# Performance work log

Hardware: AMD Instinct MI355X
Metric: run time of the kernel (lower is better)

Reference implementation:

```python
import jax, jax.numpy as jnp
import numpy as np

D_MODEL = 1024
NUM_HEADS = 16
D_FF = 4096
EPS = 1e-5


def _linear(x, w, b):
    # torch nn.Linear: y = x @ W^T + b, W is [out, in]
    return jnp.einsum('bld,od->blo', x, w) + b


def _layer_norm(x, g, b):
    mu = jnp.mean(x, axis=-1, keepdims=True)
    var = jnp.mean(jnp.square(x - mu), axis=-1, keepdims=True)
    return (x - mu) / jnp.sqrt(var + EPS) * g + b


def _mha(q, k, v, wq, bq, wk, bk, wv, bv, wo, bo, mask, num_heads):
    B, Lq, D = q.shape
    hd = D // num_heads
    Q = _linear(q, wq, bq).reshape(B, Lq, num_heads, hd).transpose(0, 2, 1, 3)
    K = _linear(k, wk, bk).reshape(B, -1, num_heads, hd).transpose(0, 2, 1, 3)
    V = _linear(v, wv, bv).reshape(B, -1, num_heads, hd).transpose(0, 2, 1, 3)
    scale = jnp.sqrt(jnp.asarray(hd, dtype=q.dtype))
    energy = jnp.einsum('bhqd,bhkd->bhqk', Q, K) / scale  # [B,H,Lq,Lk]
    energy = jnp.where(mask, energy, jnp.asarray(-1e10, dtype=q.dtype))
    attn = jax.nn.softmax(energy, axis=-1)
    x = jnp.einsum('bhqk,bhkd->bhqd', attn, V)
    x = x.transpose(0, 2, 1, 3).reshape(B, Lq, D)
    return _linear(x, wo, bo), attn


def setup_inputs() -> dict:
    key = jax.random.key(0)
    ks = iter(jax.random.split(key, 40))
    B, T, S, D, F = 4, 1024, 1024, D_MODEL, D_FF
    inp = {
        'tgt': jax.random.normal(next(ks), (B, T, D), dtype=jnp.float32),
        'enc_src': jax.random.normal(next(ks), (B, S, D), dtype=jnp.float32),
        'tgt_mask': jnp.tril(jnp.ones((1, 1, T, T), dtype=bool)),
        'src_mask': jnp.ones((1, 1, 1, S), dtype=bool),
    }
    def lin(kk, o, i):
        return jax.random.normal(kk, (o, i), dtype=jnp.float32) * 0.02
    for pfx in ('sa', 'ca'):  # self-attn and cross-attn params
        for nm in ('q', 'k', 'v', 'o'):
            inp[f'{pfx}_w{nm}'] = lin(next(ks), D, D)
            inp[f'{pfx}_b{nm}'] = jnp.zeros((D,), dtype=jnp.float32)
    inp['ff_w1'] = lin(next(ks), F, D)
    inp['ff_b1'] = jnp.zeros((F,), dtype=jnp.float32)
    inp['ff_w2'] = lin(next(ks), D, F)
    inp['ff_b2'] = jnp.zeros((D,), dtype=jnp.float32)
    for i in (1, 2, 3):
        inp[f'ln{i}_g'] = jnp.ones((D,), dtype=jnp.float32)
        inp[f'ln{i}_b'] = jnp.zeros((D,), dtype=jnp.float32)
    return inp


def reference(tgt, enc_src, tgt_mask, src_mask,
              sa_wq, sa_bq, sa_wk, sa_bk, sa_wv, sa_bv, sa_wo, sa_bo,
              ca_wq, ca_bq, ca_wk, ca_bk, ca_wv, ca_bv, ca_wo, ca_bo,
              ff_w1, ff_b1, ff_w2, ff_b2,
              ln1_g, ln1_b, ln2_g, ln2_b, ln3_g, ln3_b):
    # dropout in eval mode (identity)
    _t, _ = _mha(tgt, tgt, tgt, sa_wq, sa_bq, sa_wk, sa_bk, sa_wv, sa_bv,
                 sa_wo, sa_bo, tgt_mask, NUM_HEADS)
    tgt = _layer_norm(tgt + _t, ln1_g, ln1_b)
    _t, attention = _mha(tgt, enc_src, enc_src, ca_wq, ca_bq, ca_wk, ca_bk,
                         ca_wv, ca_bv, ca_wo, ca_bo, src_mask, NUM_HEADS)
    tgt = _layer_norm(tgt + _t, ln2_g, ln2_b)
    _t = _linear(jax.nn.relu(_linear(tgt, ff_w1, ff_b1)), ff_w2, ff_b2)
    tgt = _layer_norm(tgt + _t, ln3_g, ln3_b)
    return tgt, attention
```

## Files before the change

### kernel.cpp

```cpp
#include <hip/hip_runtime.h>
#include <hip/hip_bf16.h>

#define BBATCH 4
#define TT 1024
#define SS 1024
#define DD 1024
#define HH 16
#define HD 64
#define FFD 4096
#define MM (BBATCH*TT)

using f32x4  = __attribute__((ext_vector_type(4))) float;
using s16x8  = __attribute__((ext_vector_type(8))) short;
using bf16x8 = __attribute__((ext_vector_type(8))) __bf16;

__device__ __forceinline__ unsigned short f2b(float f) {
  union { float f; unsigned int u; } x{f};
  unsigned int r = x.u + 0x7FFFu + ((x.u >> 16) & 1u);
  return (unsigned short)(r >> 16);
}

__device__ __forceinline__ void gload16(const void* g, void* l) {
  __builtin_amdgcn_global_load_lds(
      (const __attribute__((address_space(1))) void*)g,
      (__attribute__((address_space(3))) void*)l, 16, 0, 0);
}

__device__ __forceinline__ f32x4 mfma_bf16(s16x8 a, s16x8 b, f32x4 c) {
  return __builtin_amdgcn_mfma_f32_16x16x32_bf16(
      __builtin_bit_cast(bf16x8, a), __builtin_bit_cast(bf16x8, b), c, 0, 0, 0);
}

template <int JT>
__device__ __forceinline__ void gemm_core(
    const unsigned short* __restrict__ Ab, int lda,
    const unsigned short* __restrict__ Bb, int ldb,
    int K, unsigned short* As, unsigned short* Bs, f32x4 (&acc)[4][JT])
{
  const int tid = threadIdx.x, wave = tid >> 6, lane = tid & 63;
  const int r0 = tid >> 2, c0 = (tid & 3) * 8;
  const int wrow = (wave >> 1) * 64, wcol = (wave & 1) * 16 * JT;
  const int q = lane >> 4, rl = lane & 15;
  const s16x8* Av = (const s16x8*)As;
  const s16x8* Bv = (const s16x8*)Bs;

  for (int k0 = 0; k0 < K; k0 += 32) {
    gload16(Ab + (size_t)r0 * lda + k0 + c0, As + wave * 512);
    gload16(Ab + (size_t)(r0 + 64) * lda + k0 + c0, As + wave * 512 + 2048);
    gload16(Bb + (size_t)r0 * ldb + k0 + c0, Bs + wave * 512);
    if (JT == 4)
      gload16(Bb + (size_t)(r0 + 64) * ldb + k0 + c0, Bs + wave * 512 + 2048);
    __syncthreads();
    s16x8 af[4], bfr[JT];
#pragma unroll
    for (int t = 0; t < 4; t++) af[t] = Av[(wrow + t * 16 + rl) * 4 + q];
#pragma unroll
    for (int t = 0; t < JT; t++) bfr[t] = Bv[(wcol + t * 16 + rl) * 4 + q];
#pragma unroll
    for (int i = 0; i < 4; i++)
#pragma unroll
      for (int j = 0; j < JT; j++)
        acc[i][j] = mfma_bf16(af[i], bfr[j], acc[i][j]);
    __syncthreads();
  }
}

template <int EPI, int JT>
__global__ __launch_bounds__(256) void gemm_bt(
    const unsigned short* __restrict__ A, int lda,
    const unsigned short* __restrict__ B, int ldb,
    const float* __restrict__ bias, const float* __restrict__ res,
    float* __restrict__ Cf, unsigned short* __restrict__ Cb, int ldc, int K)
{
  __shared__ __align__(16) unsigned short As[128 * 32];
  __shared__ __align__(16) unsigned short Bs[JT * 1024];
  const int bm = blockIdx.y, bn = blockIdx.x;
  const int lane = threadIdx.x & 63, wave = threadIdx.x >> 6;
  const int wrow = (wave >> 1) * 64, wcol = (wave & 1) * 16 * JT;
  const int q = lane >> 4, rl = lane & 15;

  f32x4 acc[4][JT];
  f32x4 z = {0.f, 0.f, 0.f, 0.f};
#pragma unroll
  for (int i = 0; i < 4; i++)
#pragma unroll
    for (int j = 0; j < JT; j++) acc[i][j] = z;

  gemm_core<JT>(A + (size_t)bm * 128 * lda, lda,
                B + (size_t)bn * (32 * JT) * ldb, ldb, K, As, Bs, acc);

#pragma unroll
  for (int i = 0; i < 4; i++) {
    int gm0 = bm * 128 + wrow + i * 16 + q * 4;
#pragma unroll
    for (int j = 0; j < JT; j++) {
      int gn = bn * (32 * JT) + wcol + j * 16 + rl;
      float bv = bias[gn];
#pragma unroll
      for (int r = 0; r < 4; r++) {
        size_t off = (size_t)(gm0 + r) * ldc + gn;
        float v = acc[i][j][r];
        if constexpr (EPI == 0) Cb[off] = f2b(v + bv);
        else if constexpr (EPI == 2) Cf[off] = v + bv + res[off];
        else Cb[off] = f2b(fmaxf(v + bv, 0.f));
      }
    }
  }
}

__device__ __forceinline__ void sblock_qk(
    const unsigned short* Qs, const unsigned short* Ks,
    int wrow, int wcol, int q, int rl, f32x4 (&acc)[4][4])
{
  const s16x8* Qv = (const s16x8*)Qs;
  const s16x8* Kv = (const s16x8*)Ks;
  f32x4 z = {0.f, 0.f, 0.f, 0.f};
#pragma unroll
  for (int i = 0; i < 4; i++)
#pragma unroll
    for (int j = 0; j < 4; j++) acc[i][j] = z;
#pragma unroll
  for (int kq = 0; kq < 2; kq++) {
    s16x8 af[4], bf[4];
#pragma unroll
    for (int t = 0; t < 4; t++) af[t] = Qv[kq * 512 + (wrow + t * 16 + rl) * 4 + q];
#pragma unroll
    for (int t = 0; t < 4; t++) bf[t] = Kv[kq * 512 + (wcol + t * 16 + rl) * 4 + q];
#pragma unroll
    for (int i = 0; i < 4; i++)
#pragma unroll
      for (int j = 0; j < 4; j++)
        acc[i][j] = mfma_bf16(af[i], bf[j], acc[i][j]);
  }
}

template <bool CAUSAL, bool WRITE_P>
__global__ __launch_bounds__(256, 2) void flash_attn(
    const unsigned short* __restrict__ Qg, int ldq,
    const unsigned short* __restrict__ Kg, int ldk,
    const unsigned short* __restrict__ Vt,
    float* __restrict__ Pout,
    unsigned short* __restrict__ Og)
{
  __shared__ __align__(16) unsigned short Qs[2 * 128 * 32];
  __shared__ __align__(16) unsigned short KP[4 * 128 * 40];
  __shared__ __align__(16) unsigned short Vs[4 * 64 * 32];
  __shared__ float red[2][128];

  const int tid = threadIdx.x, wave = tid >> 6, lane = tid & 63;
  const int q = lane >> 4, rl = lane & 15;
  const int bm = blockIdx.x, bh = blockIdx.y, b = bh >> 4, h = bh & 15;
  const int wrow = (wave >> 1) * 64, wcol = (wave & 1) * 64;
  const int r0 = tid >> 2, c0 = (tid & 3) * 8;

  const unsigned short* Qbase = Qg + ((size_t)b * TT + bm * 128) * ldq + h * HD;
  const unsigned short* Kbase = Kg + (size_t)b * SS * ldk + h * HD;
  const unsigned short* Vbase = Vt + ((size_t)bh << 16);

#pragma unroll
  for (int kq = 0; kq < 2; kq++) {
    gload16(Qbase + (size_t)r0 * ldq + kq * 32 + c0, Qs + kq * 4096 + wave * 512);
    gload16(Qbase + (size_t)(r0 + 64) * ldq + kq * 32 + c0, Qs + kq * 4096 + wave * 512 + 2048);
  }
  const int nch = CAUSAL ? bm + 1 : 8;
  const float NEG = -3.0e38f;

  float m_run[4][4], l_run[4][4];
#pragma unroll
  for (int i = 0; i < 4; i++)
#pragma unroll
    for (int r = 0; r < 4; r++) { m_run[i][r] = NEG; l_run[i][r] = 0.f; }

  for (int c = 0; c < nch; c++) {
    const unsigned short* src = Kbase + (size_t)c * 128 * ldk;
#pragma unroll
    for (int kq = 0; kq < 2; kq++) {
      gload16(src + (size_t)r0 * ldk + kq * 32 + c0, KP + kq * 4096 + wave * 512);
      gload16(src + (size_t)(r0 + 64) * ldk + kq * 32 + c0, KP + kq * 4096 + wave * 512 + 2048);
    }
    __syncthreads();
    f32x4 acc[4][4];
    sblock_qk(Qs, KP, wrow, wcol, q, rl, acc);
#pragma unroll
    for (int i = 0; i < 4; i++)
#pragma unroll
      for (int j = 0; j < 4; j++)
#pragma unroll
        for (int r = 0; r < 4; r++) {
          float v = acc[i][j][r] * 0.125f;
          if (CAUSAL && c == bm && (wcol + j * 16 + rl) > (wrow + i * 16 + q * 4 + r)) v = NEG;
          acc[i][j][r] = v;
        }
    float mx[4][4];
#pragma unroll
    for (int i = 0; i < 4; i++)
#pragma unroll
      for (int r = 0; r < 4; r++) {
        float m0 = fmaxf(fmaxf(acc[i][0][r], acc[i][1][r]), fmaxf(acc[i][2][r], acc[i][3][r]));
#pragma unroll
        for (int off = 1; off < 16; off <<= 1) m0 = fmaxf(m0, __shfl_xor(m0, off));
        mx[i][r] = m0;
      }
    if (rl == 0) {
#pragma unroll
      for (int i = 0; i < 4; i++)
#pragma unroll
        for (int r = 0; r < 4; r++)
          red[wave & 1][wrow + i * 16 + q * 4 + r] = mx[i][r];
    }
    __syncthreads();
    float mn[4][4];
#pragma unroll
    for (int i = 0; i < 4; i++)
#pragma unroll
      for (int r = 0; r < 4; r++) {
        int row = wrow + i * 16 + q * 4 + r;
        mn[i][r] = fmaxf(m_run[i][r], fmaxf(red[0][row], red[1][row]));
      }
    float cs[4][4];
#pragma unroll
    for (int i = 0; i < 4; i++)
#pragma unroll
      for (int r = 0; r < 4; r++) {
        float s = __expf(acc[i][0][r] - mn[i][r]) + __expf(acc[i][1][r] - mn[i][r]) +
                  __expf(acc[i][2][r] - mn[i][r]) + __expf(acc[i][3][r] - mn[i][r]);
#pragma unroll
        for (int off = 1; off < 16; off <<= 1) s += __shfl_xor(s, off);
        cs[i][r] = s;
      }
    __syncthreads();
    if (rl == 0) {
#pragma unroll
      for (int i = 0; i < 4; i++)
#pragma unroll
        for (int r = 0; r < 4; r++)
          red[wave & 1][wrow + i * 16 + q * 4 + r] = cs[i][r];
    }
    __syncthreads();
#pragma unroll
    for (int i = 0; i < 4; i++)
#pragma unroll
      for (int r = 0; r < 4; r++) {
        int row = wrow + i * 16 + q * 4 + r;
        float tot = red[0][row] + red[1][row];
        l_run[i][r] = l_run[i][r] * __expf(m_run[i][r] - mn[i][r]) + tot;
        m_run[i][r] = mn[i][r];
      }
    __syncthreads();
  }

  float invl[4][4];
#pragma unroll
  for (int i = 0; i < 4; i++)
#pragma unroll
    for (int r = 0; r < 4; r++) invl[i][r] = 1.0f / l_run[i][r];

  const int wc2 = (wave & 1) * 32;
  f32x4 oacc[4][2];
  f32x4 z = {0.f, 0.f, 0.f, 0.f};
#pragma unroll
  for (int i = 0; i < 4; i++) { oacc[i][0] = z; oacc[i][1] = z; }

  for (int c = 0; c < nch; c++) {
    __syncthreads();
    const unsigned short* src = Kbase + (size_t)c * 128 * ldk;
#pragma unroll
    for (int kq = 0; kq < 2; kq++) {
      gload16(src + (size_t)r0 * ldk + kq * 32 + c0, KP + kq * 4096 + wave * 512);
      gload16(src + (size_t)(r0 + 64) * ldk + kq * 32 + c0, KP + kq * 4096 + wave * 512 + 2048);
    }
#pragma unroll
    for (int ks = 0; ks < 4; ks++)
      gload16(Vbase + (size_t)r0 * SS + c * 128 + ks * 32 + c0, Vs + ks * 2048 + wave * 512);
    __syncthreads();
    f32x4 acc[4][4];
    sblock_qk(Qs, KP, wrow, wcol, q, rl, acc);
#pragma unroll
    for (int i = 0; i < 4; i++)
#pragma unroll
      for (int j = 0; j < 4; j++)
#pragma unroll
        for (int r = 0; r < 4; r++) {
          float v = acc[i][j][r] * 0.125f;
          bool msk = CAUSAL && c == bm && (wcol + j * 16 + rl) > (wrow + i * 16 + q * 4 + r);
          acc[i][j][r] = msk ? 0.f : __expf(v - m_run[i][r]) * invl[i][r];
        }
    if (WRITE_P) {
      float* Pb = Pout + ((size_t)bh << 20) +
                  ((size_t)(bm * 128 + wrow + q * 4) << 10) + c * 128 + wcol + rl;
#pragma unroll
      for (int i = 0; i < 4; i++)
#pragma unroll
        for (int r = 0; r < 4; r++)
#pragma unroll
          for (int j = 0; j < 4; j++)
            Pb[(size_t)((i * 16 + r) << 10) + j * 16] = acc[i][j][r];
    }
    __syncthreads();
#pragma unroll
    for (int i = 0; i < 4; i++)
#pragma unroll
      for (int j = 0; j < 4; j++) {
        int col = wcol + j * 16 + rl;
        int ks = col >> 5, cc = col & 31;
#pragma unroll
        for (int r = 0; r < 4; r++)
          KP[ks * 5120 + (wrow + i * 16 + q * 4 + r) * 40 + cc] = f2b(acc[i][j][r]);
      }
    __syncthreads();
    const s16x8* Pv = (const s16x8*)KP;
    const s16x8* Vv = (const s16x8*)Vs;
#pragma unroll
    for (int ks = 0; ks < 4; ks++) {
      s16x8 af[4], bf[2];
#pragma unroll
      for (int t = 0; t < 4; t++) af[t] = Pv[ks * 640 + (wrow + t * 16 + rl) * 5 + q];
#pragma unroll
      for (int t = 0; t < 2; t++) bf[t] = Vv[ks * 256 + (wc2 + t * 16 + rl) * 4 + q];
#pragma unroll
      for (int i = 0; i < 4; i++)
#pragma unroll
        for (int jt = 0; jt < 2; jt++)
          oacc[i][jt] = mfma_bf16(af[i], bf[jt], oacc[i][jt]);
    }
  }

#pragma unroll
  for (int i = 0; i < 4; i++)
#pragma unroll
    for (int jt = 0; jt < 2; jt++)
#pragma unroll
      for (int r = 0; r < 4; r++) {
        int row = bm * 128 + wrow + i * 16 + q * 4 + r;
        int col = h * HD + wc2 + jt * 16 + rl;
        Og[((size_t)b * TT + row) * DD + col] = f2b(oacc[i][jt][r]);
      }
}

__global__ __launch_bounds__(256) void transpose_v(
    const unsigned short* __restrict__ V, int ldv, unsigned short* __restrict__ Vt)
{
  __shared__ unsigned short tile[64][68];
  const int bh = blockIdx.z, b = bh >> 4, h = bh & 15;
  const int s0 = blockIdx.x * 64;
  const int tid = threadIdx.x;
#pragma unroll
  for (int i = 0; i < 4; i++) {
    int idx = i * 256 + tid;
    int sl = idx >> 4, d0 = (idx & 15) * 4;
    ushort4 v = *(const ushort4*)&V[((size_t)b * SS + s0 + sl) * ldv + h * HD + d0];
    tile[sl][d0] = v.x; tile[sl][d0 + 1] = v.y; tile[sl][d0 + 2] = v.z; tile[sl][d0 + 3] = v.w;
  }
  __syncthreads();
#pragma unroll
  for (int i = 0; i < 4; i++) {
    int idx = i * 256 + tid;
    int d = idx >> 4, s4 = (idx & 15) * 4;
    ushort4 o = make_ushort4(tile[s4][d], tile[s4 + 1][d], tile[s4 + 2][d], tile[s4 + 3][d]);
    *(ushort4*)&Vt[((size_t)bh * HD + d) * SS + s0 + s4] = o;
  }
}

__global__ __launch_bounds__(256) void ln_k(
    const float* __restrict__ src, const float* __restrict__ g,
    const float* __restrict__ b, float* __restrict__ dstf,
    unsigned short* __restrict__ dstb)
{
  __shared__ float sh[10];
  const size_t row = blockIdx.x;
  const int tid = threadIdx.x;
  float4 v = ((const float4*)(src + (row << 10)))[tid];
  float s = v.x + v.y + v.z + v.w;
  float ss = v.x * v.x + v.y * v.y + v.z * v.z + v.w * v.w;
  for (int o = 32; o; o >>= 1) { s += __shfl_down(s, o); ss += __shfl_down(ss, o); }
  if ((tid & 63) == 0) { sh[tid >> 6] = s; sh[4 + (tid >> 6)] = ss; }
  __syncthreads();
  if (tid == 0) {
    sh[8] = sh[0] + sh[1] + sh[2] + sh[3];
    sh[9] = sh[4] + sh[5] + sh[6] + sh[7];
  }
  __syncthreads();
  const float mean = sh[8] * (1.0f / DD);
  const float var = sh[9] * (1.0f / DD) - mean * mean;
  const float inv = rsqrtf(var + 1e-5f);
  float4 gv = ((const float4*)g)[tid];
  float4 bv = ((const float4*)b)[tid];
  float4 y;
  y.x = (v.x - mean) * inv * gv.x + bv.x;
  y.y = (v.y - mean) * inv * gv.y + bv.y;
  y.z = (v.z - mean) * inv * gv.z + bv.z;
  y.w = (v.w - mean) * inv * gv.w + bv.w;
  if (dstf) ((float4*)(dstf + (row << 10)))[tid] = y;
  if (dstb) {
    ushort4 o = make_ushort4(f2b(y.x), f2b(y.y), f2b(y.z), f2b(y.w));
    ((ushort4*)(dstb + (row << 10)))[tid] = o;
  }
}

__global__ __launch_bounds__(256) void cvt_k(
    const float* __restrict__ src, unsigned short* __restrict__ dst, int n4)
{
  int i = blockIdx.x * 256 + threadIdx.x;
  if (i < n4) {
    float4 v = ((const float4*)src)[i];
    ushort4 o = make_ushort4(f2b(v.x), f2b(v.y), f2b(v.z), f2b(v.w));
    ((ushort4*)dst)[i] = o;
  }
}

__global__ __launch_bounds__(256) void bias_pack(
    const float* __restrict__ bq, const float* __restrict__ bk, const float* __restrict__ bv,
    const float* __restrict__ bk2, const float* __restrict__ bv2,
    float* __restrict__ bqkv, float* __restrict__ bkv)
{
  int i = blockIdx.x * 256 + threadIdx.x;
  if (i < 1024) bqkv[i] = bq[i];
  else if (i < 2048) bqkv[i] = bk[i - 1024];
  else if (i < 3072) bqkv[i] = bv[i - 2048];
  else if (i < 4096) bkv[i - 3072] = bk2[i - 3072];
  else if (i < 5120) bkv[i - 3072] = bv2[i - 4096 + 1024];
}


extern "C" void kernel_launch(void* const* d_in, const int* in_sizes, int n_in,
                              void* d_out, int out_size, void* d_ws, size_t ws_size,
                              hipStream_t stream)
{
  const float* tgt = (const float*)d_in[0];
  const float* enc = (const float*)d_in[1];
  const float* sa_wq = (const float*)d_in[4];  const float* sa_bq = (const float*)d_in[5];
  const float* sa_wk = (const float*)d_in[6];  const float* sa_bk = (const float*)d_in[7];
  const float* sa_wv = (const float*)d_in[8];  const float* sa_bv = (const float*)d_in[9];
  const float* sa_wo = (const float*)d_in[10]; const float* sa_bo = (const float*)d_in[11];
  const float* ca_wq = (const float*)d_in[12]; const float* ca_bq = (const float*)d_in[13];
  const float* ca_wk = (const float*)d_in[14]; const float* ca_bk = (const float*)d_in[15];
  const float* ca_wv = (const float*)d_in[16]; const float* ca_bv = (const float*)d_in[17];
  const float* ca_wo = (const float*)d_in[18]; const float* ca_bo = (const float*)d_in[19];
  const float* ff_w1 = (const float*)d_in[20]; const float* ff_b1 = (const float*)d_in[21];
  const float* ff_w2 = (const float*)d_in[22]; const float* ff_b2 = (const float*)d_in[23];
  const float* ln1_g = (const float*)d_in[24]; const float* ln1_b = (const float*)d_in[25];
  const float* ln2_g = (const float*)d_in[26]; const float* ln2_b = (const float*)d_in[27];
  const float* ln3_g = (const float*)d_in[28]; const float* ln3_b = (const float*)d_in[29];

  float* out_tgt = (float*)d_out;
  float* out_attn = (float*)d_out + (size_t)MM * DD;

  char* w = (char*)d_ws;
  size_t off = 0;
  auto alloc = [&](size_t bytes) { void* p = w + off; off += (bytes + 255) & ~(size_t)255; return p; };
  unsigned short* Xb   = (unsigned short*)alloc((size_t)MM * DD * 2);
  unsigned short* Eb   = (unsigned short*)alloc((size_t)MM * DD * 2);
  unsigned short* Wq1  = (unsigned short*)alloc((size_t)DD * DD * 2);
  unsigned short* Wk1  = (unsigned short*)alloc((size_t)DD * DD * 2);
  unsigned short* Wv1  = (unsigned short*)alloc((size_t)DD * DD * 2);
  unsigned short* Wo1  = (unsigned short*)alloc((size_t)DD * DD * 2);
  unsigned short* Wq2  = (unsigned short*)alloc((size_t)DD * DD * 2);
  unsigned short* Wk2  = (unsigned short*)alloc((size_t)DD * DD * 2);
  unsigned short* Wv2  = (unsigned short*)alloc((size_t)DD * DD * 2);
  unsigned short* Wo2  = (unsigned short*)alloc((size_t)DD * DD * 2);
  unsigned short* Wf1  = (unsigned short*)alloc((size_t)FFD * DD * 2);
  unsigned short* Wf2  = (unsigned short*)alloc((size_t)DD * FFD * 2);
  unsigned short* QKVb = (unsigned short*)alloc((size_t)MM * 3 * DD * 2);
  unsigned short* KVb  = (unsigned short*)alloc((size_t)MM * 2 * DD * 2);
  unsigned short* Qca  = (unsigned short*)alloc((size_t)MM * DD * 2);
  unsigned short* Vt   = (unsigned short*)alloc((size_t)MM * DD * 2);
  unsigned short* Ob   = (unsigned short*)alloc((size_t)MM * DD * 2);
  float*          res1 = (float*)alloc((size_t)MM * DD * 4);
  unsigned short* t1b  = (unsigned short*)alloc((size_t)MM * DD * 2);
  float*          res2 = (float*)alloc((size_t)MM * DD * 4);
  unsigned short* t2b  = (unsigned short*)alloc((size_t)MM * DD * 2);
  unsigned short* Fb   = (unsigned short*)alloc((size_t)MM * FFD * 2);
  float*          bqkv = (float*)alloc(3072 * 4);
  float*          bkv  = (float*)alloc(2048 * 4);

  auto cvt = [&](const float* s, unsigned short* d, int n) {
    cvt_k<<<n / 1024, 256, 0, stream>>>(s, d, n / 4);
  };

  bias_pack<<<20, 256, 0, stream>>>(sa_bq, sa_bk, sa_bv, ca_bk, ca_bv, bqkv, bkv);
  cvt(tgt, Xb, MM * DD);
  cvt(enc, Eb, MM * DD);
  cvt(sa_wq, Wq1, DD * DD); cvt(sa_wk, Wk1, DD * DD);
  cvt(sa_wv, Wv1, DD * DD); cvt(sa_wo, Wo1, DD * DD);
  cvt(ca_wq, Wq2, DD * DD); cvt(ca_wk, Wk2, DD * DD);
  cvt(ca_wv, Wv2, DD * DD); cvt(ca_wo, Wo2, DD * DD);
  cvt(ff_w1, Wf1, FFD * DD); cvt(ff_w2, Wf2, DD * FFD);

  const dim3 gQKV(24, 32);
  const dim3 gKV(16, 32);
  const dim3 gN64(16, 32);
  const dim3 gFF1(32, 32);
  const dim3 gFl(8, 64);
  const dim3 gTr(SS / 64, 1, BBATCH * HH);

  gemm_bt<0, 4><<<gQKV, 256, 0, stream>>>(Xb, DD, Wq1, DD, bqkv, nullptr, nullptr, QKVb, 3 * DD, DD);
  transpose_v<<<gTr, 256, 0, stream>>>(QKVb + 2 * DD, 3 * DD, Vt);
  flash_attn<true, false><<<gFl, 256, 0, stream>>>(QKVb, 3 * DD, QKVb + DD, 3 * DD, Vt, nullptr, Ob);
  gemm_bt<2, 2><<<gN64, 256, 0, stream>>>(Ob, DD, Wo1, DD, sa_bo, tgt, res1, nullptr, DD, DD);
  ln_k<<<MM, 256, 0, stream>>>(res1, ln1_g, ln1_b, res1, t1b);

  gemm_bt<0, 2><<<gN64, 256, 0, stream>>>(t1b, DD, Wq2, DD, ca_bq, nullptr, nullptr, Qca, DD, DD);
  gemm_bt<0, 4><<<gKV, 256, 0, stream>>>(Eb, DD, Wk2, DD, bkv, nullptr, nullptr, KVb, 2 * DD, DD);
  transpose_v<<<gTr, 256, 0, stream>>>(KVb + DD, 2 * DD, Vt);
  flash_attn<false, true><<<gFl, 256, 0, stream>>>(Qca, DD, KVb, 2 * DD, Vt, out_attn, Ob);
  gemm_bt<2, 2><<<gN64, 256, 0, stream>>>(Ob, DD, Wo2, DD, ca_bo, res1, res2, nullptr, DD, DD);
  ln_k<<<MM, 256, 0, stream>>>(res2, ln2_g, ln2_b, res2, t2b);

  gemm_bt<3, 4><<<gFF1, 256, 0, stream>>>(t2b, DD, Wf1, DD, ff_b1, nullptr, nullptr, Fb, FFD, DD);
  gemm_bt<2, 2><<<gN64, 256, 0, stream>>>(Fb, FFD, Wf2, FFD, ff_b2, res2, res1, nullptr, DD, FFD);
  ln_k<<<MM, 256, 0, stream>>>(res1, ln3_g, ln3_b, out_tgt, nullptr);
}
```

Baseline: 904.1 us.

## Add single-pass online-softmax causal attention kernel and merge conversion launches

Adds a dedicated causal self-attention kernel that computes softmax online in one pass over key chunks, rescaling the running output accumulator. It does not write the probability matrix. This replaces the generic flash_attn path for self-attention, which may have used multiple passes. The twelve separate fp32-to-bf16 conversion launches are also merged into one kernel that selects its source buffer from a table of offsets, cutting launch overhead.

```diff
diff --git a/kernel.cpp b/kernel.cpp
--- a/kernel.cpp
+++ b/kernel.cpp
@@ -132,6 +132,176 @@
       for (int j = 0; j < 4; j++)
         acc[i][j] = mfma_bf16(af[i], bf[j], acc[i][j]);
   }
+}
+
+__global__ __launch_bounds__(256, 2) void flash_sa(
+    const unsigned short* __restrict__ Qg, int ldq,
+    const unsigned short* __restrict__ Kg, int ldk,
+    const unsigned short* __restrict__ Vt,
+    unsigned short* __restrict__ Og)
+{
+  __shared__ __align__(16) unsigned short Qs[2 * 128 * 32];
+  __shared__ __align__(16) unsigned short KP[4 * 128 * 40];
+  __shared__ __align__(16) unsigned short Vs[4 * 64 * 32];
+  __shared__ float red[2][128];
+
+  const int tid = threadIdx.x, wave = tid >> 6, lane = tid & 63;
+  const int q = lane >> 4, rl = lane & 15;
+  const int bm = blockIdx.x, bh = blockIdx.y, b = bh >> 4, h = bh & 15;
+  const int wrow = (wave >> 1) * 64, wcol = (wave & 1) * 64;
+  const int wc2 = (wave & 1) * 32;
+  const int r0 = tid >> 2, c0 = (tid & 3) * 8;
+
+  const unsigned short* Qbase = Qg + ((size_t)b * TT + bm * 128) * ldq + h * HD;
+  const unsigned short* Kbase = Kg + (size_t)b * SS * ldk + h * HD;
+  const unsigned short* Vbase = Vt + ((size_t)bh << 16);
+
+#pragma unroll
+  for (int kq = 0; kq < 2; kq++) {
+    gload16(Qbase + (size_t)r0 * ldq + kq * 32 + c0, Qs + kq * 4096 + wave * 512);
+    gload16(Qbase + (size_t)(r0 + 64) * ldq + kq * 32 + c0, Qs + kq * 4096 + wave * 512 + 2048);
+  }
+  const int nch = bm + 1;
+  const float NEG = -3.0e38f;
+
+  float m_run[4][4], l_run[4][4];
+  f32x4 oacc[4][2];
+  f32x4 z = {0.f, 0.f, 0.f, 0.f};
+#pragma unroll
+  for (int i = 0; i < 4; i++) {
+    oacc[i][0] = z; oacc[i][1] = z;
+#pragma unroll
+    for (int r = 0; r < 4; r++) { m_run[i][r] = NEG; l_run[i][r] = 0.f; }
+  }
+
+  for (int c = 0; c < nch; c++) {
+    const unsigned short* src = Kbase + (size_t)c * 128 * ldk;
+#pragma unroll
+    for (int kq = 0; kq < 2; kq++) {
+      gload16(src + (size_t)r0 * ldk + kq * 32 + c0, KP + kq * 4096 + wave * 512);
+      gload16(src + (size_t)(r0 + 64) * ldk + kq * 32 + c0, KP + kq * 4096 + wave * 512 + 2048);
+    }
+#pragma unroll
+    for (int ks = 0; ks < 4; ks++)
+      gload16(Vbase + (size_t)r0 * SS + c * 128 + ks * 32 + c0, Vs + ks * 2048 + wave * 512);
+    __syncthreads();
+
+    f32x4 acc[4][4];
+    sblock_qk(Qs, KP, wrow, wcol, q, rl, acc);
+#pragma unroll
+    for (int i = 0; i < 4; i++)
+#pragma unroll
+      for (int j = 0; j < 4; j++)
+#pragma unroll
+        for (int r = 0; r < 4; r++) {
+          float v = acc[i][j][r] * 0.125f;
+          if (c == bm && (wcol + j * 16 + rl) > (wrow + i * 16 + q * 4 + r)) v = NEG;
+          acc[i][j][r] = v;
+        }
+    float mx[4][4];
+#pragma unroll
+    for (int i = 0; i < 4; i++)
+#pragma unroll
+      for (int r = 0; r < 4; r++) {
+        float m0 = fmaxf(fmaxf(acc[i][0][r], acc[i][1][r]), fmaxf(acc[i][2][r], acc[i][3][r]));
+#pragma unroll
+        for (int off = 1; off < 16; off <<= 1) m0 = fmaxf(m0, __shfl_xor(m0, off));
+        mx[i][r] = m0;
+      }
+    if (rl == 0) {
+#pragma unroll
+      for (int i = 0; i < 4; i++)
+#pragma unroll
+        for (int r = 0; r < 4; r++)
+          red[wave & 1][wrow + i * 16 + q * 4 + r] = mx[i][r];
+    }
+    __syncthreads();
+    float mn[4][4];
+#pragma unroll
+    for (int i = 0; i < 4; i++)
+#pragma unroll
+      for (int r = 0; r < 4; r++) {
+        int row = wrow + i * 16 + q * 4 + r;
+        mn[i][r] = fmaxf(m_run[i][r], fmaxf(red[0][row], red[1][row]));
+      }
+    float cs[4][4];
+#pragma unroll
+    for (int i = 0; i < 4; i++)
+#pragma unroll
+      for (int r = 0; r < 4; r++) {
+#pragma unroll
+        for (int j = 0; j < 4; j++) acc[i][j][r] = __expf(acc[i][j][r] - mn[i][r]);
+        float s = acc[i][0][r] + acc[i][1][r] + acc[i][2][r] + acc[i][3][r];
+#pragma unroll
+        for (int off = 1; off < 16; off <<= 1) s += __shfl_xor(s, off);
+        cs[i][r] = s;
+      }
+    __syncthreads();
+    if (rl == 0) {
+#pragma unroll
+      for (int i = 0; i < 4; i++)
+#pragma unroll
+        for (int r = 0; r < 4; r++)
+          red[wave & 1][wrow + i * 16 + q * 4 + r] = cs[i][r];
+    }
+    __syncthreads();
+#pragma unroll
+    for (int i = 0; i < 4; i++)
+#pragma unroll
+      for (int r = 0; r < 4; r++) {
+        int row = wrow + i * 16 + q * 4 + r;
+        float tot = red[0][row] + red[1][row];
+        float al = __expf(m_run[i][r] - mn[i][r]);
+        l_run[i][r] = l_run[i][r] * al + tot;
+        m_run[i][r] = mn[i][r];
+        oacc[i][0][r] *= al;
+        oacc[i][1][r] *= al;
+      }
+#pragma unroll
+    for (int i = 0; i < 4; i++)
+#pragma unroll
+      for (int j = 0; j < 4; j++) {
+        int col = wcol + j * 16 + rl;
+        int ks = col >> 5, cc = col & 31;
+#pragma unroll
+        for (int r = 0; r < 4; r++)
+          KP[ks * 5120 + (wrow + i * 16 + q * 4 + r) * 40 + cc] = f2b(acc[i][j][r]);
+      }
+    __syncthreads();
+    const s16x8* Pv = (const s16x8*)KP;
+    const s16x8* Vv = (const s16x8*)Vs;
+#pragma unroll
+    for (int ks = 0; ks < 4; ks++) {
+      s16x8 af[4], bf[2];
+#pragma unroll
+      for (int t = 0; t < 4; t++) af[t] = Pv[ks * 640 + (wrow + t * 16 + rl) * 5 + q];
+#pragma unroll
+      for (int t = 0; t < 2; t++) bf[t] = Vv[ks * 256 + (wc2 + t * 16 + rl) * 4 + q];
+#pragma unroll
+      for (int i = 0; i < 4; i++)
+#pragma unroll
+        for (int jt = 0; jt < 2; jt++)
+          oacc[i][jt] = mfma_bf16(af[i], bf[jt], oacc[i][jt]);
+    }
+    __syncthreads();
+  }
+
+  float invl[4][4];
+#pragma unroll
+  for (int i = 0; i < 4; i++)
+#pragma unroll
+    for (int r = 0; r < 4; r++) invl[i][r] = 1.0f / l_run[i][r];
+
+#pragma unroll
+  for (int i = 0; i < 4; i++)
+#pragma unroll
+    for (int jt = 0; jt < 2; jt++)
+#pragma unroll
+      for (int r = 0; r < 4; r++) {
+        int row = bm * 128 + wrow + i * 16 + q * 4 + r;
+        int col = h * HD + wc2 + jt * 16 + rl;
+        Og[((size_t)b * TT + row) * DD + col] = f2b(oacc[i][jt][r] * invl[i][r]);
+      }
 }
 
 template <bool CAUSAL, bool WRITE_P>
@@ -397,15 +567,23 @@
   }
 }
 
-__global__ __launch_bounds__(256) void cvt_k(
-    const float* __restrict__ src, unsigned short* __restrict__ dst, int n4)
-{
+struct CvtArgs {
+  const float* src[12];
+  unsigned short* dst[12];
+};
+
+__global__ __launch_bounds__(256) void cvt_all(CvtArgs a) {
+  constexpr int st[13] = {0,       1048576, 2097152, 2359296, 2621440,
+                          2883584, 3145728, 3407872, 3670016, 3932160,
+                          4194304, 5242880, 6291456};
   int i = blockIdx.x * 256 + threadIdx.x;
-  if (i < n4) {
-    float4 v = ((const float4*)src)[i];
-    ushort4 o = make_ushort4(f2b(v.x), f2b(v.y), f2b(v.z), f2b(v.w));
-    ((ushort4*)dst)[i] = o;
-  }
+  int s = 0;
+#pragma unroll
+  for (int k = 1; k < 12; k++) s += (i >= st[k]) ? 1 : 0;
+  int j = i - st[s];
+  float4 v = ((const float4*)a.src[s])[j];
+  ushort4 o = make_ushort4(f2b(v.x), f2b(v.y), f2b(v.z), f2b(v.w));
+  ((ushort4*)a.dst[s])[j] = o;
 }
 
 __global__ __launch_bounds__(256) void bias_pack(
@@ -473,18 +651,22 @@
   float*          bqkv = (float*)alloc(3072 * 4);
   float*          bkv  = (float*)alloc(2048 * 4);
 
-  auto cvt = [&](const float* s, unsigned short* d, int n) {
-    cvt_k<<<n / 1024, 256, 0, stream>>>(s, d, n / 4);
-  };
+  CvtArgs ca;
+  ca.src[0] = tgt;   ca.dst[0] = Xb;
+  ca.src[1] = enc;   ca.dst[1] = Eb;
+  ca.src[2] = sa_wq; ca.dst[2] = Wq1;
+  ca.src[3] = sa_wk; ca.dst[3] = Wk1;
+  ca.src[4] = sa_wv; ca.dst[4] = Wv1;
+  ca.src[5] = sa_wo; ca.dst[5] = Wo1;
+  ca.src[6] = ca_wq; ca.dst[6] = Wq2;
+  ca.src[7] = ca_wk; ca.dst[7] = Wk2;
+  ca.src[8] = ca_wv; ca.dst[8] = Wv2;
+  ca.src[9] = ca_wo; ca.dst[9] = Wo2;
+  ca.src[10] = ff_w1; ca.dst[10] = Wf1;
+  ca.src[11] = ff_w2; ca.dst[11] = Wf2;
 
   bias_pack<<<20, 256, 0, stream>>>(sa_bq, sa_bk, sa_bv, ca_bk, ca_bv, bqkv, bkv);
-  cvt(tgt, Xb, MM * DD);
-  cvt(enc, Eb, MM * DD);
-  cvt(sa_wq, Wq1, DD * DD); cvt(sa_wk, Wk1, DD * DD);
-  cvt(sa_wv, Wv1, DD * DD); cvt(sa_wo, Wo1, DD * DD);
-  cvt(ca_wq, Wq2, DD * DD); cvt(ca_wk, Wk2, DD * DD);
-  cvt(ca_wv, Wv2, DD * DD); cvt(ca_wo, Wo2, DD * DD);
-  cvt(ff_w1, Wf1, FFD * DD); cvt(ff_w2, Wf2, DD * FFD);
+  cvt_all<<<24576, 256, 0, stream>>>(ca);
 
   const dim3 gQKV(24, 32);
   const dim3 gKV(16, 32);
@@ -495,7 +677,7 @@
 
   gemm_bt<0, 4><<<gQKV, 256, 0, stream>>>(Xb, DD, Wq1, DD, bqkv, nullptr, nullptr, QKVb, 3 * DD, DD);
   transpose_v<<<gTr, 256, 0, stream>>>(QKVb + 2 * DD, 3 * DD, Vt);
-  flash_attn<true, false><<<gFl, 256, 0, stream>>>(QKVb, 3 * DD, QKVb + DD, 3 * DD, Vt, nullptr, Ob);
+  flash_sa<<<gFl, 256, 0, stream>>>(QKVb, 3 * DD, QKVb + DD, 3 * DD, Vt, Ob);
   gemm_bt<2, 2><<<gN64, 256, 0, stream>>>(Ob, DD, Wo1, DD, sa_bo, tgt, res1, nullptr, DD, DD);
   ln_k<<<MM, 256, 0, stream>>>(res1, ln1_g, ln1_b, res1, t1b);
 
```

Result: faster. 866.4 us (-4.2%).
